# Kernel optimization log

Measured on AMD Instinct MI355X. Metric: run time of the kernel, lower is better.

The kernel has to match this reference:

```python
import jax, jax.numpy as jnp
import numpy as np
from jax import lax


def _lstm_cell(x, h, c, W_ih, W_hh, b_ih, b_hh):
    # torch nn.LSTMCell: gates = x W_ih^T + b_ih + h W_hh^T + b_hh, order i,f,g,o
    gates = x @ W_ih.T + h @ W_hh.T + (b_ih + b_hh)
    i, f, g, o = jnp.split(gates, 4, axis=-1)
    c_new = jax.nn.sigmoid(f) * c + jax.nn.sigmoid(i) * jnp.tanh(g)
    h_new = jax.nn.sigmoid(o) * jnp.tanh(c_new)
    return h_new, c_new


def setup_inputs():
    key = jax.random.key(0)
    ks = jax.random.split(key, 10)
    B, S, E, H, V = 128, 20, 512, 512, 10000
    images = jax.random.normal(ks[0], (B, E), jnp.float32)
    captions = jax.random.randint(ks[1], (B, S), 0, V)
    length = jax.random.randint(ks[2], (B, 1), 2, S + 1)
    length = length.at[0, 0].set(S)  # guarantee max decode length == S-1 (static shape)
    s = 0.05
    emb = jax.random.normal(ks[3], (V, E), jnp.float32) * s
    W_ih = jax.random.normal(ks[4], (4 * H, E), jnp.float32) * s
    W_hh = jax.random.normal(ks[5], (4 * H, H), jnp.float32) * s
    b_ih = jax.random.normal(ks[6], (4 * H,), jnp.float32) * s
    b_hh = jax.random.normal(ks[7], (4 * H,), jnp.float32) * s
    fc_w = jax.random.normal(ks[8], (V, H), jnp.float32) * s
    fc_b = jax.random.normal(ks[9], (V,), jnp.float32) * s
    return dict(images=images, captions=captions, length=length, emb=emb,
                W_ih=W_ih, W_hh=W_hh, b_ih=b_ih, b_hh=b_hh, fc_w=fc_w, fc_b=fc_b)


def reference(images, captions, length, emb, W_ih, W_hh, b_ih, b_hh, fc_w, fc_b):
    B, S = captions.shape
    T = S - 1  # static max(decode_lengths) by construction
    H = W_hh.shape[1]
    lens = length[:, 0]
    sort_ind = jnp.argsort(-lens)  # stable descending sort, like torch .sort(descending=True)
    sorted_lens = lens[sort_ind]
    dec_len = sorted_lens - 1
    features = images[sort_ind]
    captions_s = captions[sort_ind]
    embeddings = emb[captions_s]  # [B, S, E]

    zeros = jnp.zeros((B, H), images.dtype)
    h, c = _lstm_cell(features, zeros, zeros, W_ih, W_hh, b_ih, b_hh)

    xs = (jnp.swapaxes(embeddings[:, :T, :], 0, 1), jnp.arange(T))  # [T,B,E], [T]

    def step(carry, x):
        h, c = carry
        x_t, t = x
        # ragged batch in the original == masking here: rows with dec_len<=t never
        # contribute to any future valid output (lengths sorted descending).
        h, c = _lstm_cell(x_t, h, c, W_ih, W_hh, b_ih, b_hh)
        preds = h @ fc_w.T + fc_b  # dropout is identity in eval mode
        preds = jnp.where((dec_len > t)[:, None], preds, 0.0)
        return (h, c), preds

    (_, _), preds = lax.scan(step, (h, c), xs)
    predictions = jnp.swapaxes(preds, 0, 1)  # [B, T, V]
    return predictions, captions_s, dec_len, sort_ind
```

## Files before the change

### kernel.cpp

```cpp
#include <hip/hip_runtime.h>

typedef float  f32x4 __attribute__((ext_vector_type(4)));
typedef short  s16x8 __attribute__((ext_vector_type(8)));
typedef unsigned short u16x4 __attribute__((ext_vector_type(4)));

#define MFMA16(a,b,c) __builtin_amdgcn_mfma_f32_16x16x32_bf16(a,b,c,0,0,0)

#define PRED_ELEMS 24320000ull

__device__ __forceinline__ unsigned short f2bf(float f){
  unsigned u = __builtin_bit_cast(unsigned, f);
  u += 0x7fffu + ((u >> 16) & 1u);
  return (unsigned short)(u >> 16);
}
__device__ __forceinline__ float sigf(float x){ return 1.0f/(1.0f + __expf(-x)); }
__device__ __forceinline__ float tanh_(float x){
  x = fminf(15.0f, fmaxf(-15.0f, x));
  float e = __expf(2.0f*x);
  return (e - 1.0f) / (e + 1.0f);
}
__device__ __forceinline__ s16x8 ld8(const unsigned short* p){
  return *reinterpret_cast<const s16x8*>(p);
}
__device__ __forceinline__ void gload_lds16(const unsigned short* src, unsigned short* dst){
  __builtin_amdgcn_global_load_lds(
      (const __attribute__((address_space(1))) void*)src,
      (__attribute__((address_space(3))) void*)dst, 16, 0, 0);
}

__global__ void k0_sort(const int* __restrict__ length, const int* __restrict__ captions,
                        float* __restrict__ out, int* __restrict__ sortp,
                        int* __restrict__ nactp, unsigned int* __restrict__ cnt4k)
{
  __shared__ int sl[128], sdl[128], ssi[128];
  int tid = threadIdx.x;
  for (int k = tid; k < 1024; k += 128) cnt4k[k] = 0u;
  if (tid < 128) sl[tid] = length[tid];
  __syncthreads();
  if (tid < 128){
    int l = sl[tid];
    int rank = 0;
    for (int j = 0; j < 128; ++j){
      int lj = sl[j];
      rank += (lj > l) || (lj == l && j < tid);
    }
    sortp[rank] = tid;
    ssi[rank] = tid;   sdl[rank] = l - 1;
  }
  __syncthreads();
  if (tid < 20){
    int c = 0;
    for (int r = 0; r < 128; ++r) c += (sdl[r] >= tid);
    nactp[tid] = c;
  }
  if (tid < 128){
    const size_t P = PRED_ELEMS;
    int si = ssi[tid];
    for (int t = 0; t < 20; ++t) out[P + tid*20 + t] = (float)captions[si*20 + t];
    out[P + 2560 + tid] = (float)sdl[tid];
    out[P + 2688 + tid] = (float)si;
  }
}

__device__ __forceinline__ void cvt4(unsigned short* dst, const float* src, int u){
  f32x4 v = *reinterpret_cast<const f32x4*>(src + (size_t)u*4);
  u16x4 o;
  o[0]=f2bf(v[0]); o[1]=f2bf(v[1]); o[2]=f2bf(v[2]); o[3]=f2bf(v[3]);
  *reinterpret_cast<u16x4*>(dst + (size_t)u*4) = o;
}

__global__ void k1_convert(const float* __restrict__ images, const int* __restrict__ captions,
    const float* __restrict__ emb, const float* __restrict__ wih, const float* __restrict__ whh,
    const float* __restrict__ bih, const float* __restrict__ bhh, const float* __restrict__ fcw,
    const int* __restrict__ sortp,
    unsigned short* __restrict__ wihb, unsigned short* __restrict__ whhb,
    unsigned short* __restrict__ fcwb, float* __restrict__ biasp,
    unsigned short* __restrict__ xseq, unsigned short* __restrict__ hseq,
    unsigned short* __restrict__ hloc)
{
  const int U0 = 262144;
  const int U1 = 262144;
  const int U2 = 1294336;
  const int U3 = 512;
  const int U4 = 327680;
  const int U5 = 16384;
  const int U6 = 16384;
  const int total = U0+U1+U2+U3+U4+U5+U6;
  for (int i = blockIdx.x*blockDim.x + threadIdx.x; i < total; i += gridDim.x*blockDim.x){
    int j = i;
    if (j < U0){ cvt4(wihb, wih, j); continue; }
    j -= U0;
    if (j < U1){ cvt4(whhb, whh, j); continue; }
    j -= U1;
    if (j < U2){
      int row = j >> 7;
      if (row < 10000) cvt4(fcwb, fcw, j);
      else { u16x4 z = {0,0,0,0}; *reinterpret_cast<u16x4*>(fcwb + (size_t)j*4) = z; }
      continue;
    }
    j -= U2;
    if (j < U3){
      int e0 = j*4;
      for (int e = 0; e < 4; ++e) biasp[e0+e] = bih[e0+e] + bhh[e0+e];
      continue;
    }
    j -= U3;
    if (j < U4){
      int elem = j*4;
      int s = elem >> 16;
      int rem = elem & 65535;
      int r = rem >> 9;
      int k = rem & 511;
      const float* src;
      if (s == 0) src = images + (size_t)sortp[r]*512 + k;
      else {
        int cap = captions[sortp[r]*20 + (s-1)];
        src = emb + (size_t)cap*512 + k;
      }
      f32x4 v = *reinterpret_cast<const f32x4*>(src);
      u16x4 o;
      o[0]=f2bf(v[0]); o[1]=f2bf(v[1]); o[2]=f2bf(v[2]); o[3]=f2bf(v[3]);
      *reinterpret_cast<u16x4*>(xseq + (size_t)j*4) = o;
      continue;
    }
    j -= U4;
    if (j < U5){ u16x4 z = {0,0,0,0}; *reinterpret_cast<u16x4*>(hseq + (size_t)j*4) = z; continue; }
    j -= U5;
    {
      int e0 = j*4;
      int x = e0 >> 13;
      int rem = e0 & 8191;
      u16x4 z = {0,0,0,0};
      *reinterpret_cast<u16x4*>(hloc + (size_t)x*172032 + rem) = z;
    }
  }
}

__global__ __launch_bounds__(256) void k2_gx(
    const unsigned short* __restrict__ xseq, const unsigned short* __restrict__ wihb,
    const float* __restrict__ biasp, float* __restrict__ gx)
{
  const int lane = threadIdx.x & 63;
  const int wv   = threadIdx.x >> 6;
  const int wr   = wv >> 1, wc = wv & 1;
  const int fr   = lane & 15;
  const int fk   = (lane >> 4) * 8;
  const int s    = blockIdx.y;
  const int g0   = blockIdx.x * 128;
  const unsigned short* A = xseq + (size_t)s*65536;

  f32x4 acc[4][4];
  for (int i = 0; i < 4; ++i)
    for (int j = 0; j < 4; ++j)
      acc[i][j] = (f32x4){0.f,0.f,0.f,0.f};

  #pragma unroll 4
  for (int k0 = 0; k0 < 512; k0 += 32){
    s16x8 a[4], b[4];
    for (int i = 0; i < 4; ++i)
      a[i] = ld8(A + (wr*64 + i*16 + fr)*512 + k0 + fk);
    for (int j = 0; j < 4; ++j)
      b[j] = ld8(wihb + (size_t)(g0 + wc*64 + j*16 + fr)*512 + k0 + fk);
    for (int i = 0; i < 4; ++i)
      for (int j = 0; j < 4; ++j)
        acc[i][j] = MFMA16(a[i], b[j], acc[i][j]);
  }

  const int rr = (lane >> 4) * 4;
  for (int j = 0; j < 4; ++j){
    int g = g0 + wc*64 + j*16 + fr;
    float bb = biasp[g];
    for (int i = 0; i < 4; ++i)
      for (int p = 0; p < 4; ++p){
        int r = wr*64 + i*16 + rr + p;
        gx[((size_t)s*128 + r)*2048 + g] = acc[i][j][p] + bb;
      }
  }
}

__global__ __launch_bounds__(256) void lstm_chain(
    const float* __restrict__ gx, const unsigned short* __restrict__ whh,
    unsigned short* __restrict__ hseq, unsigned short* __restrict__ hloc,
    const int* __restrict__ nact, unsigned int* __restrict__ claimc,
    unsigned int* __restrict__ flags)
{
  const int tid = threadIdx.x;
  __shared__ int s_xw;
  __shared__ unsigned short Wl[64*524];
  __shared__ float pg[4][4][16][17];

  if (tid == 0){
    unsigned xcc;
    asm volatile("s_getreg_b32 %0, hwreg(20, 0, 4)" : "=s"(xcc));
    int x = (int)(xcc & 7u);
    unsigned slot = __hip_atomic_fetch_add(claimc + x*64, 1u,
                      __ATOMIC_RELAXED, __HIP_MEMORY_SCOPE_AGENT);
    s_xw = (x << 8) | (int)(slot & 255u);
  }
  __syncthreads();
  const int x = s_xw >> 8;
  const int w = s_xw & 255;
  if (w >= 32) return;
  const int R0 = x*16;
  const int C0 = w*16;
  unsigned int* myflags = flags + x*64;

  const int lane = tid & 63;
  const int kk   = tid >> 6;
  const int fr   = lane & 15;
  const int fkq  = (lane >> 4) * 8;

  for (int idx = tid; idx < 64*64; idx += 256){
    int lr = idx >> 6, kc = (idx & 63)*8;
    int q = lr >> 4, jj = lr & 15;
    s16x8 v = ld8(whh + (size_t)(q*512 + C0 + jj)*512 + kc);
    *reinterpret_cast<s16x8*>(&Wl[lr*524 + kc]) = v;
  }

  unsigned short* hl = hloc + (size_t)x*172032;
  const int prow = tid >> 4;
  const int pcol = tid & 15;
  float creg = 0.f;
  __syncthreads();

  for (int s = 0; s < 20; ++s){
    if (R0 >= nact[s]) break;
    const unsigned short* hp = hl + (size_t)s*8192;

    s16x8 a[4];
    #pragma unroll
    for (int i = 0; i < 4; ++i)
      a[i] = ld8(hp + fr*512 + kk*128 + i*32 + fkq);
    const float* gxr = gx + ((size_t)s*128 + R0 + prow)*2048 + C0 + pcol;
    float gvi = gxr[0], gvf = gxr[512], gvg = gxr[1024], gvo = gxr[1536];

    #pragma unroll
    for (int q = 0; q < 4; ++q){
      f32x4 acc = (f32x4){0.f,0.f,0.f,0.f};
      #pragma unroll
      for (int i = 0; i < 4; ++i){
        s16x8 b = *reinterpret_cast<const s16x8*>(&Wl[(q*16 + fr)*524 + kk*128 + i*32 + fkq]);
        acc = MFMA16(a[i], b, acc);
      }
      const int rr = (lane >> 4) * 4;
      #pragma unroll
      for (int p = 0; p < 4; ++p)
        pg[kk][q][rr + p][fr] = acc[p];
    }
    __syncthreads();

    {
      float iv = pg[0][0][prow][pcol] + pg[1][0][prow][pcol]
               + pg[2][0][prow][pcol] + pg[3][0][prow][pcol] + gvi;
      float fv = pg[0][1][prow][pcol] + pg[1][1][prow][pcol]
               + pg[2][1][prow][pcol] + pg[3][1][prow][pcol] + gvf;
      float gv = pg[0][2][prow][pcol] + pg[1][2][prow][pcol]
               + pg[2][2][prow][pcol] + pg[3][2][prow][pcol] + gvg;
      float ov = pg[0][3][prow][pcol] + pg[1][3][prow][pcol]
               + pg[2][3][prow][pcol] + pg[3][3][prow][pcol] + gvo;
      creg = sigf(fv)*creg + sigf(iv)*tanh_(gv);
      float h = sigf(ov)*tanh_(creg);
      unsigned short hb = f2bf(h);
      hl[(size_t)(s+1)*8192 + prow*512 + C0 + pcol] = hb;
      hseq[(size_t)(s+1)*65536 + (R0 + prow)*512 + C0 + pcol] = hb;
    }
    __syncthreads();

    if (s < 19 && nact[s+1] > R0){
      const unsigned tgt = (unsigned)(s + 1);
      if (tid == 0)
        __hip_atomic_store(&myflags[w], tgt, __ATOMIC_RELAXED, __HIP_MEMORY_SCOPE_AGENT);
      if (tid < 64){
        long guard = 0;
        for (;;){
          bool ok = true;
          if (tid < 32)
            ok = (__hip_atomic_load(&myflags[tid], __ATOMIC_RELAXED,
                                    __HIP_MEMORY_SCOPE_AGENT) >= tgt);
          if (__all(ok) || ++guard > (1L << 20)) break;
          __builtin_amdgcn_s_sleep(1);
        }
      }
      __syncthreads();
    }
  }
}

__global__ __launch_bounds__(256) void fc_kernel(
    const unsigned short* __restrict__ hseq, const unsigned short* __restrict__ fcwb,
    const float* __restrict__ fcb, const int* __restrict__ nact,
    float* __restrict__ out)
{
  const int b    = blockIdx.x;
  const int x    = b & 7;
  const int slot = b >> 3;
  const int t    = slot % 19;
  const int p    = x + 8*(slot/19);
  if (p >= 79) return;
  const int v0   = p * 128;
  const int tid  = threadIdx.x;

  __shared__ unsigned short Ab[2][128*64];
  __shared__ unsigned short Bb[2][128*64];

  const unsigned short* Ag = hseq + (size_t)(t + 2)*65536;
  const unsigned short* Bg = fcwb + (size_t)v0*512;
  const int n_t = nact[t + 1];

  const int srow = tid >> 3;
  const int sphy = tid & 7;
  const int wuni = (tid >> 6) << 9;

  #define STAGE(gsrc, lbuf, kt)                                              \
    _Pragma("unroll")                                                        \
    for (int call = 0; call < 4; ++call){                                    \
      int row_ = call*32 + srow;                                             \
      gload_lds16(gsrc + (size_t)row_*512 + (kt)*64 + ((sphy ^ (row_ & 7)) << 3), \
                  lbuf + call*2048 + wuni);                                  \
    }

  const int lane = tid & 63;
  const int wv   = tid >> 6;
  const int wr   = wv >> 1, wc = wv & 1;
  const int fr   = lane & 15;
  const int hi   = lane >> 4;

  f32x4 acc[4][4];
  #pragma unroll
  for (int i = 0; i < 4; ++i)
    #pragma unroll
    for (int j = 0; j < 4; ++j)
      acc[i][j] = (f32x4){0.f,0.f,0.f,0.f};

  STAGE(Ag, Ab[0], 0)
  STAGE(Bg, Bb[0], 0)
  asm volatile("s_waitcnt vmcnt(0)" ::: "memory");
  __syncthreads();

  int cur = 0;
  for (int kt = 0; kt < 8; ++kt){
    if (kt < 7){
      STAGE(Ag, Ab[cur^1], kt+1)
      STAGE(Bg, Bb[cur^1], kt+1)
    }
    const unsigned short* As = Ab[cur];
    const unsigned short* Bs = Bb[cur];
    #pragma unroll
    for (int kk = 0; kk < 2; ++kk){
      const int c = kk*4 + hi;
      s16x8 af[4], bf[4];
      #pragma unroll
      for (int i = 0; i < 4; ++i){
        int row = wr*64 + i*16 + fr;
        af[i] = ld8(As + row*64 + ((c ^ (row & 7)) << 3));
      }
      #pragma unroll
      for (int j = 0; j < 4; ++j){
        int col = wc*64 + j*16 + fr;
        bf[j] = ld8(Bs + col*64 + ((c ^ (col & 7)) << 3));
      }
      #pragma unroll
      for (int i = 0; i < 4; ++i)
        #pragma unroll
        for (int j = 0; j < 4; ++j)
          acc[i][j] = MFMA16(af[i], bf[j], acc[i][j]);
    }
    asm volatile("s_waitcnt vmcnt(0)" ::: "memory");
    __syncthreads();
    cur ^= 1;
  }

  const int rr = hi * 4;
  #pragma unroll
  for (int j = 0; j < 4; ++j){
    int v = v0 + wc*64 + j*16 + fr;
    if (v >= 10000) continue;
    float bb = fcb[v];
    #pragma unroll
    for (int i = 0; i < 4; ++i){
      #pragma unroll
      for (int pp = 0; pp < 4; ++pp){
        int r = wr*64 + i*16 + rr + pp;
        out[(size_t)(r*19 + t)*10000 + v] = (r < n_t) ? (acc[i][j][pp] + bb) : 0.0f;
      }
    }
  }
  #undef STAGE
}

extern "C" void kernel_launch(void* const* d_in, const int* in_sizes, int n_in,
                              void* d_out, int out_size, void* d_ws, size_t ws_size,
                              hipStream_t stream) {
  const float* images   = (const float*)d_in[0];
  const int*   captions = (const int*)  d_in[1];
  const int*   length   = (const int*)  d_in[2];
  const float* emb      = (const float*)d_in[3];
  const float* W_ih     = (const float*)d_in[4];
  const float* W_hh     = (const float*)d_in[5];
  const float* b_ih     = (const float*)d_in[6];
  const float* b_hh     = (const float*)d_in[7];
  const float* fc_w     = (const float*)d_in[8];
  const float* fc_b     = (const float*)d_in[9];
  float* out = (float*)d_out;
  char*  ws  = (char*)d_ws;

  int*            sortp  = (int*)           (ws + 0);
  int*            nactp  = (int*)           (ws + 2048);
  float*          biasp  = (float*)         (ws + 4096);
  unsigned int*   cnt4k  = (unsigned int*)  (ws + 12288);
  unsigned int*   claimc = cnt4k;
  unsigned int*   flags  = cnt4k + 512;
  unsigned short* hloc   = (unsigned short*)(ws + 16384);
  unsigned short* hseq   = (unsigned short*)(ws + 2768896);
  unsigned short* xseq   = (unsigned short*)(ws + 5521408);
  unsigned short* wihb   = (unsigned short*)(ws + 8142848);
  unsigned short* whhb   = (unsigned short*)(ws + 10240000);
  unsigned short* fcwb   = (unsigned short*)(ws + 12337152);
  float*          gx     = (float*)         (ws + 22691840);

  k0_sort<<<1, 128, 0, stream>>>(length, captions, out, sortp, nactp, cnt4k);
  k1_convert<<<4096, 256, 0, stream>>>(images, captions, emb, W_ih, W_hh, b_ih, b_hh,
                                       fc_w, sortp, wihb, whhb, fcwb, biasp, xseq, hseq, hloc);
  k2_gx<<<dim3(16, 20), 256, 0, stream>>>(xseq, wihb, biasp, gx);
  lstm_chain<<<256, 256, 0, stream>>>(gx, whhb, hseq, hloc, nactp, claimc, flags);
  fc_kernel<<<1520, 256, 0, stream>>>(hseq, fcwb, fc_b, nactp, out);
}
```

Before: 148.9 us.

## Fuse input-gate projection into the recurrent LSTM chain kernel

Removes the separate k2_gx GEMM kernel and its fp32 gx buffer. Each LSTM chain block now also keeps its W_ih slice in LDS and computes x·W_ih^T with extra MFMAs per step, adding the bias from registers. This saves a kernel launch and the gx write/read traffic, but lengthens the serial per-step critical path with twice the MFMA work and an extra global load of x. The hseq store is also moved after the barrier.

```diff
diff --git a/kernel.cpp b/kernel.cpp
--- a/kernel.cpp
+++ b/kernel.cpp
@@ -136,57 +136,17 @@
   }
 }
 
-__global__ __launch_bounds__(256) void k2_gx(
-    const unsigned short* __restrict__ xseq, const unsigned short* __restrict__ wihb,
-    const float* __restrict__ biasp, float* __restrict__ gx)
-{
-  const int lane = threadIdx.x & 63;
-  const int wv   = threadIdx.x >> 6;
-  const int wr   = wv >> 1, wc = wv & 1;
-  const int fr   = lane & 15;
-  const int fk   = (lane >> 4) * 8;
-  const int s    = blockIdx.y;
-  const int g0   = blockIdx.x * 128;
-  const unsigned short* A = xseq + (size_t)s*65536;
-
-  f32x4 acc[4][4];
-  for (int i = 0; i < 4; ++i)
-    for (int j = 0; j < 4; ++j)
-      acc[i][j] = (f32x4){0.f,0.f,0.f,0.f};
-
-  #pragma unroll 4
-  for (int k0 = 0; k0 < 512; k0 += 32){
-    s16x8 a[4], b[4];
-    for (int i = 0; i < 4; ++i)
-      a[i] = ld8(A + (wr*64 + i*16 + fr)*512 + k0 + fk);
-    for (int j = 0; j < 4; ++j)
-      b[j] = ld8(wihb + (size_t)(g0 + wc*64 + j*16 + fr)*512 + k0 + fk);
-    for (int i = 0; i < 4; ++i)
-      for (int j = 0; j < 4; ++j)
-        acc[i][j] = MFMA16(a[i], b[j], acc[i][j]);
-  }
-
-  const int rr = (lane >> 4) * 4;
-  for (int j = 0; j < 4; ++j){
-    int g = g0 + wc*64 + j*16 + fr;
-    float bb = biasp[g];
-    for (int i = 0; i < 4; ++i)
-      for (int p = 0; p < 4; ++p){
-        int r = wr*64 + i*16 + rr + p;
-        gx[((size_t)s*128 + r)*2048 + g] = acc[i][j][p] + bb;
-      }
-  }
-}
-
 __global__ __launch_bounds__(256) void lstm_chain(
-    const float* __restrict__ gx, const unsigned short* __restrict__ whh,
+    const unsigned short* __restrict__ xseq, const unsigned short* __restrict__ wih,
+    const unsigned short* __restrict__ whh, const float* __restrict__ biasp,
     unsigned short* __restrict__ hseq, unsigned short* __restrict__ hloc,
     const int* __restrict__ nact, unsigned int* __restrict__ claimc,
     unsigned int* __restrict__ flags)
 {
   const int tid = threadIdx.x;
   __shared__ int s_xw;
-  __shared__ unsigned short Wl[64*524];
+  __shared__ unsigned short WIl[64*524];
+  __shared__ unsigned short WHl[64*524];
   __shared__ float pg[4][4][16][17];
 
   if (tid == 0){
@@ -213,34 +173,42 @@
   for (int idx = tid; idx < 64*64; idx += 256){
     int lr = idx >> 6, kc = (idx & 63)*8;
     int q = lr >> 4, jj = lr & 15;
-    s16x8 v = ld8(whh + (size_t)(q*512 + C0 + jj)*512 + kc);
-    *reinterpret_cast<s16x8*>(&Wl[lr*524 + kc]) = v;
+    size_t off = (size_t)(q*512 + C0 + jj)*512 + kc;
+    *reinterpret_cast<s16x8*>(&WIl[lr*524 + kc]) = ld8(wih + off);
+    *reinterpret_cast<s16x8*>(&WHl[lr*524 + kc]) = ld8(whh + off);
   }
 
   unsigned short* hl = hloc + (size_t)x*172032;
   const int prow = tid >> 4;
   const int pcol = tid & 15;
+  const float bz0 = biasp[       C0 + pcol];
+  const float bz1 = biasp[ 512 + C0 + pcol];
+  const float bz2 = biasp[1024 + C0 + pcol];
+  const float bz3 = biasp[1536 + C0 + pcol];
   float creg = 0.f;
   __syncthreads();
 
   for (int s = 0; s < 20; ++s){
     if (R0 >= nact[s]) break;
     const unsigned short* hp = hl + (size_t)s*8192;
-
-    s16x8 a[4];
-    #pragma unroll
-    for (int i = 0; i < 4; ++i)
-      a[i] = ld8(hp + fr*512 + kk*128 + i*32 + fkq);
-    const float* gxr = gx + ((size_t)s*128 + R0 + prow)*2048 + C0 + pcol;
-    float gvi = gxr[0], gvf = gxr[512], gvg = gxr[1024], gvo = gxr[1536];
+    const unsigned short* xp = xseq + (size_t)s*65536;
+
+    s16x8 ah[4], ax[4];
+    #pragma unroll
+    for (int i = 0; i < 4; ++i){
+      ah[i] = ld8(hp + fr*512 + kk*128 + i*32 + fkq);
+      ax[i] = ld8(xp + (R0 + fr)*512 + kk*128 + i*32 + fkq);
+    }
 
     #pragma unroll
     for (int q = 0; q < 4; ++q){
       f32x4 acc = (f32x4){0.f,0.f,0.f,0.f};
       #pragma unroll
       for (int i = 0; i < 4; ++i){
-        s16x8 b = *reinterpret_cast<const s16x8*>(&Wl[(q*16 + fr)*524 + kk*128 + i*32 + fkq]);
-        acc = MFMA16(a[i], b, acc);
+        s16x8 bi = *reinterpret_cast<const s16x8*>(&WIl[(q*16 + fr)*524 + kk*128 + i*32 + fkq]);
+        s16x8 bh = *reinterpret_cast<const s16x8*>(&WHl[(q*16 + fr)*524 + kk*128 + i*32 + fkq]);
+        acc = MFMA16(ax[i], bi, acc);
+        acc = MFMA16(ah[i], bh, acc);
       }
       const int rr = (lane >> 4) * 4;
       #pragma unroll
@@ -249,22 +217,24 @@
     }
     __syncthreads();
 
+    unsigned short hb;
     {
       float iv = pg[0][0][prow][pcol] + pg[1][0][prow][pcol]
-               + pg[2][0][prow][pcol] + pg[3][0][prow][pcol] + gvi;
+               + pg[2][0][prow][pcol] + pg[3][0][prow][pcol] + bz0;
       float fv = pg[0][1][prow][pcol] + pg[1][1][prow][pcol]
-               + pg[2][1][prow][pcol] + pg[3][1][prow][pcol] + gvf;
+               + pg[2][1][prow][pcol] + pg[3][1][prow][pcol] + bz1;
       float gv = pg[0][2][prow][pcol] + pg[1][2][prow][pcol]
-               + pg[2][2][prow][pcol] + pg[3][2][prow][pcol] + gvg;
+               + pg[2][2][prow][pcol] + pg[3][2][prow][pcol] + bz2;
       float ov = pg[0][3][prow][pcol] + pg[1][3][prow][pcol]
-               + pg[2][3][prow][pcol] + pg[3][3][prow][pcol] + gvo;
+               + pg[2][3][prow][pcol] + pg[3][3][prow][pcol] + bz3;
       creg = sigf(fv)*creg + sigf(iv)*tanh_(gv);
       float h = sigf(ov)*tanh_(creg);
-      unsigned short hb = f2bf(h);
+      hb = f2bf(h);
       hl[(size_t)(s+1)*8192 + prow*512 + C0 + pcol] = hb;
-      hseq[(size_t)(s+1)*65536 + (R0 + prow)*512 + C0 + pcol] = hb;
     }
     __syncthreads();
+
+    hseq[(size_t)(s+1)*65536 + (R0 + prow)*512 + C0 + pcol] = hb;
 
     if (s < 19 && nact[s+1] > R0){
       const unsigned tgt = (unsigned)(s + 1);
@@ -416,12 +386,11 @@
   unsigned short* wihb   = (unsigned short*)(ws + 8142848);
   unsigned short* whhb   = (unsigned short*)(ws + 10240000);
   unsigned short* fcwb   = (unsigned short*)(ws + 12337152);
-  float*          gx     = (float*)         (ws + 22691840);
 
   k0_sort<<<1, 128, 0, stream>>>(length, captions, out, sortp, nactp, cnt4k);
   k1_convert<<<4096, 256, 0, stream>>>(images, captions, emb, W_ih, W_hh, b_ih, b_hh,
                                        fc_w, sortp, wihb, whhb, fcwb, biasp, xseq, hseq, hloc);
-  k2_gx<<<dim3(16, 20), 256, 0, stream>>>(xseq, wihb, biasp, gx);
-  lstm_chain<<<256, 256, 0, stream>>>(gx, whhb, hseq, hloc, nactp, claimc, flags);
+  lstm_chain<<<256, 256, 0, stream>>>(xseq, wihb, whhb, biasp, hseq, hloc,
+                                      nactp, claimc, flags);
   fc_kernel<<<1520, 256, 0, stream>>>(hseq, fcwb, fc_b, nactp, out);
 }
```

After: 127.9 us. -14.1%, faster.
